# Kernel optimization log

Measured on AMD Instinct MI355X. Metric: run time of the kernel, lower is better.

The kernel has to match this reference:

```python
import jax, jax.numpy as jnp
import numpy as np

DIM = 512
HEADS = 16
WIN = (7, 7)
N = WIN[0] * WIN[1]
B_ = 4096
HEAD_DIM = DIM // HEADS
SCALE = HEAD_DIM ** (-0.5)


def _relative_position_index():
    ch = np.arange(WIN[0])
    cw = np.arange(WIN[1])
    coords = np.stack(np.meshgrid(ch, cw, indexing='ij'))  # (2, Wh, Ww)
    cf = coords.reshape(2, -1)                               # (2, N)
    rel = cf[:, :, None] - cf[:, None, :]                    # (2, N, N)
    rel = rel.transpose(1, 2, 0).astype(np.int32)            # (N, N, 2)
    rel[:, :, 0] += WIN[0] - 1
    rel[:, :, 1] += WIN[1] - 1
    rel[:, :, 0] *= 2 * WIN[1] - 1
    return jnp.asarray(rel.sum(-1))                          # (N, N) int32


def setup_inputs() -> dict:
    key = jax.random.key(0)
    ks = jax.random.split(key, 6)
    x = jax.random.normal(ks[0], (B_, N, DIM), dtype=jnp.float32)
    qkv_w = jax.random.normal(ks[1], (3 * DIM, DIM), dtype=jnp.float32) * (DIM ** -0.5)
    qkv_b = jnp.zeros((3 * DIM,), dtype=jnp.float32)
    proj_w = jax.random.normal(ks[2], (DIM, DIM), dtype=jnp.float32) * (DIM ** -0.5)
    proj_b = jnp.zeros((DIM,), dtype=jnp.float32)
    n_rel = (2 * WIN[0] - 1) * (2 * WIN[1] - 1)  # 169
    bias_table = jax.random.normal(ks[3], (n_rel, HEADS), dtype=jnp.float32) * 0.02
    rel_idx = _relative_position_index()
    return {"x": x, "qkv_w": qkv_w, "qkv_b": qkv_b, "proj_w": proj_w,
            "proj_b": proj_b, "bias_table": bias_table, "rel_idx": rel_idx}


def reference(x, qkv_w, qkv_b, proj_w, proj_b, bias_table, rel_idx):
    B, n, C = x.shape
    # qkv projection: (B, N, 3C) -> (3, B, H, N, hd)
    qkv = x @ qkv_w.T + qkv_b
    qkv = qkv.reshape(B, n, 3, HEADS, HEAD_DIM).transpose(2, 0, 3, 1, 4)
    q, k, v = qkv[0], qkv[1], qkv[2]
    q = q * SCALE
    attn = jnp.einsum('bhnd,bhmd->bhnm', q, k)               # (B, H, N, N)
    # gather relative position bias: (N*N, H) -> (H, N, N)
    bias = bias_table[rel_idx.reshape(-1)].reshape(n, n, HEADS).transpose(2, 0, 1)
    attn = jax.nn.softmax(attn + bias[None], axis=-1)
    out = jnp.einsum('bhnm,bhmd->bhnd', attn, v)
    out = out.transpose(0, 2, 1, 3).reshape(B, n, C)
    return out @ proj_w.T + proj_b
```

## Files before the change

kernel.cpp:

```cpp
#include <hip/hip_runtime.h>
#include <cstdint>
#include <type_traits>

#define B_WIN 4096
#define NTOK 49
#define DIMC 512
#define HEADS 16
#define HD 32
#define M_ROWS (B_WIN * NTOK)
#define SCALE 0.17677669529663689f

using bf16x8 = __attribute__((ext_vector_type(8))) short;
using f32x4  = __attribute__((ext_vector_type(4))) float;
using u16x8  = __attribute__((ext_vector_type(8))) unsigned short;

__device__ inline unsigned short f2bf(float f) {
    uint32_t u = __float_as_uint(f);
    uint32_t r = (u + 0x7fffu + ((u >> 16) & 1u)) >> 16;
    return (unsigned short)r;
}
__device__ inline unsigned int pk2(float lo, float hi) {
    return (unsigned int)f2bf(lo) | ((unsigned int)f2bf(hi) << 16);
}

__device__ __forceinline__ void gll16(const unsigned short* g, unsigned short* l) {
    __builtin_amdgcn_global_load_lds(
        (const __attribute__((address_space(1))) void*)g,
        (__attribute__((address_space(3))) void*)l, 16, 0, 0);
}

#define DSR(dst, addr) asm volatile("ds_read_b128 %0, %1" : "=v"(dst) : "v"(addr))
#define SCHED0() __builtin_amdgcn_sched_barrier(0)
#define BARRIER() do { SCHED0(); __builtin_amdgcn_s_barrier(); SCHED0(); } while (0)
#define LGKM0() do { asm volatile("s_waitcnt lgkmcnt(0)"); SCHED0(); } while (0)

__global__ __launch_bounds__(256) void cvt_f32_bf16(
    const float* __restrict__ in, unsigned short* __restrict__ out, int n4)
{
    for (int i = blockIdx.x * blockDim.x + threadIdx.x; i < n4;
         i += gridDim.x * blockDim.x) {
        float4 v = reinterpret_cast<const float4*>(in)[i];
        ushort4 o;
        o.x = f2bf(v.x); o.y = f2bf(v.y); o.z = f2bf(v.z); o.w = f2bf(v.w);
        reinterpret_cast<ushort4*>(out)[i] = o;
    }
}

__global__ __launch_bounds__(256) void build_bias(
    const float* __restrict__ btab, const int* __restrict__ ridx,
    float* __restrict__ biasPad)
{
    const int idx = blockIdx.x * 256 + threadIdx.x;
    const int h = idx >> 12, rem = idx & 4095;
    const int i = rem >> 6, j = rem & 63;
    float v = -1e30f;
    if (i < NTOK && j < NTOK) v = btab[ridx[i * NTOK + j] * HEADS + h];
    biasPad[idx] = v;
}

template <int OUTF32>
__global__ __launch_bounds__(512, 2) void gemm8p(
    const unsigned short* __restrict__ A,
    const unsigned short* __restrict__ W,
    const float* __restrict__ bias,
    void* __restrict__ Craw,
    int N, int ntn)
{
    extern __shared__ unsigned short lds[];
    constexpr int K = 512, NT = 8;

    const int nwg = gridDim.x;
    const int bid = blockIdx.x;
    const int wg = (bid & 7) * (nwg >> 3) + (bid >> 3);
    const int tn = wg % ntn, tm = wg / ntn;
    const size_t m0 = (size_t)tm * 256, n0 = (size_t)tn * 256;

    const int t = threadIdx.x;
    const int lane = t & 63, wid = t >> 6;
    const int wm = wid >> 2, wn = wid & 3;
    const int l15 = lane & 15, l4 = lane >> 4;

    const unsigned short* pA[2];
    const unsigned short* pB[2];
    int dA[2], dB[2];
#pragma unroll
    for (int u = 0; u < 2; ++u) {
        const int f = t + u * 512, rl = f >> 3, c = f & 7, g = c ^ (rl & 7);
        const int lrA = (rl & 63) + (rl >> 6) * 128;
        const int lrB = ((rl >> 5) << 6) + (rl & 31);
        pA[u] = A + (m0 + lrA) * K + g * 8;
        pB[u] = W + (n0 + lrB) * K + g * 8;
        dA[u] = lrA * 64 + c * 8;
        dB[u] = 32768 + lrB * 64 + c * 8;
    }
#define STG_A(h, T) { const int _b = ((T) & 1) * 16384, _kt = (T) * 64;      \
    gll16(pA[0] + (h) * 64 * K + _kt, lds + _b + dA[0] + (h) * 4096);        \
    gll16(pA[1] + (h) * 64 * K + _kt, lds + _b + dA[1] + (h) * 4096); }
#define STG_B(h, T) { const int _b = ((T) & 1) * 16384, _kt = (T) * 64;      \
    gll16(pB[0] + (h) * 32 * K + _kt, lds + _b + dB[0] + (h) * 2048);        \
    gll16(pB[1] + (h) * 32 * K + _kt, lds + _b + dB[1] + (h) * 2048); }

    const unsigned lbase = (unsigned)(uintptr_t)lds;
    const unsigned swz = (unsigned)(l15 & 7);
    const unsigned cx0 = ((0u + l4) ^ swz) * 16u;
    const unsigned cx1 = ((4u + l4) ^ swz) * 16u;
    const unsigned arow = (unsigned)(wm * 128 + l15) * 128u;
    const unsigned brow = (unsigned)(wn * 64 + l15) * 128u;

    f32x4 acc[8][4] = {};
    bf16x8 a[4][2], b0[2][2], b1[2][2];

    STG_A(0, 0); STG_B(0, 0); STG_A(1, 0); STG_B(1, 0);
    STG_A(0, 1); STG_B(0, 1); STG_A(1, 1);
    asm volatile("s_waitcnt vmcnt(6)");
    SCHED0();
    BARRIER();

    for (int S = 0; S < NT; ++S) {
        const int bs = S & 1;
        const unsigned ab = lbase + (unsigned)bs * 32768u;
        const unsigned bb = lbase + 65536u + (unsigned)bs * 32768u;

#pragma unroll
        for (int m = 0; m < 4; ++m) {
            DSR(a[m][0], ab + arow + m * 2048u + cx0);
            DSR(a[m][1], ab + arow + m * 2048u + cx1);
        }
#pragma unroll
        for (int n = 0; n < 2; ++n) {
            DSR(b0[n][0], bb + brow + n * 2048u + cx0);
            DSR(b0[n][1], bb + brow + n * 2048u + cx1);
        }
        if (S + 1 < NT) STG_B(1, S + 1);
        BARRIER(); LGKM0();
        __builtin_amdgcn_s_setprio(1);
#pragma unroll
        for (int m = 0; m < 4; ++m)
#pragma unroll
            for (int n = 0; n < 2; ++n)
#pragma unroll
                for (int ks = 0; ks < 2; ++ks)
                    acc[m][n] = __builtin_amdgcn_mfma_f32_16x16x32_bf16(
                        a[m][ks], b0[n][ks], acc[m][n], 0, 0, 0);
        __builtin_amdgcn_s_setprio(0);
        BARRIER();

#pragma unroll
        for (int n = 0; n < 2; ++n) {
            DSR(b1[n][0], bb + brow + (n + 2) * 2048u + cx0);
            DSR(b1[n][1], bb + brow + (n + 2) * 2048u + cx1);
        }
        if (S + 2 < NT) STG_A(0, S + 2);
        BARRIER(); LGKM0();
        __builtin_amdgcn_s_setprio(1);
#pragma unroll
        for (int m = 0; m < 4; ++m)
#pragma unroll
            for (int n = 0; n < 2; ++n)
#pragma unroll
                for (int ks = 0; ks < 2; ++ks)
                    acc[m][n + 2] = __builtin_amdgcn_mfma_f32_16x16x32_bf16(
                        a[m][ks], b1[n][ks], acc[m][n + 2], 0, 0, 0);
        __builtin_amdgcn_s_setprio(0);
        BARRIER();

#pragma unroll
        for (int m = 0; m < 4; ++m) {
            DSR(a[m][0], ab + arow + 8192u + m * 2048u + cx0);
            DSR(a[m][1], ab + arow + 8192u + m * 2048u + cx1);
        }
        if (S + 2 < NT) STG_B(0, S + 2);
        BARRIER(); LGKM0();
        __builtin_amdgcn_s_setprio(1);
#pragma unroll
        for (int m = 0; m < 4; ++m)
#pragma unroll
            for (int n = 0; n < 2; ++n)
#pragma unroll
                for (int ks = 0; ks < 2; ++ks)
                    acc[m + 4][n] = __builtin_amdgcn_mfma_f32_16x16x32_bf16(
                        a[m][ks], b0[n][ks], acc[m + 4][n], 0, 0, 0);
        __builtin_amdgcn_s_setprio(0);
        BARRIER();

        if (S + 2 < NT) STG_A(1, S + 2);
        if (S < NT - 2)       { asm volatile("s_waitcnt vmcnt(6)"); SCHED0(); }
        else if (S == NT - 2) { asm volatile("s_waitcnt vmcnt(0)"); SCHED0(); }
        BARRIER();
        __builtin_amdgcn_s_setprio(1);
#pragma unroll
        for (int m = 0; m < 4; ++m)
#pragma unroll
            for (int n = 0; n < 2; ++n)
#pragma unroll
                for (int ks = 0; ks < 2; ++ks)
                    acc[m + 4][n + 2] = __builtin_amdgcn_mfma_f32_16x16x32_bf16(
                        a[m][ks], b1[n][ks], acc[m + 4][n + 2], 0, 0, 0);
        __builtin_amdgcn_s_setprio(0);
        BARRIER();
    }

#pragma unroll
    for (int m = 0; m < 8; ++m) {
#pragma unroll
        for (int n = 0; n < 4; ++n) {
            const size_t col = n0 + wn * 64 + n * 16 + l15;
            const float bv = bias[col];
#pragma unroll
            for (int r = 0; r < 4; ++r) {
                const size_t row = m0 + wm * 128 + m * 16 + l4 * 4 + r;
                const float v = acc[m][n][r] + bv;
                if constexpr (OUTF32)
                    ((float*)Craw)[row * N + col] = v;
                else
                    ((unsigned short*)Craw)[row * N + col] = f2bf(v);
            }
        }
    }
#undef STG_A
#undef STG_B
}

__global__ __launch_bounds__(256) void attn_mfma(
    const unsigned short* __restrict__ qkv,
    const float* __restrict__ biasPad,
    unsigned short* __restrict__ attn_out)
{
    __shared__ unsigned short vtile[4][32][72];

    const int w = threadIdx.x >> 6;
    const int g = blockIdx.x * 4 + w;
    const int b = g >> 4, h = g & 15;
    const int lane = threadIdx.x & 63;
    const int l15 = lane & 15, l4 = lane >> 4;

    bf16x8 aq[4], bk[4], vload[4];
#pragma unroll
    for (int mt = 0; mt < 4; ++mt) {
        const int tok = mt * 16 + l15;
        bf16x8 zq = {}, zk = {}, zv = {};
        if (tok < NTOK) {
            const unsigned short* base =
                qkv + (size_t)(b * NTOK + tok) * 1536 + h * HD + l4 * 8;
            zq = *(const bf16x8*)base;
            zk = *(const bf16x8*)(base + 512);
            zv = *(const bf16x8*)(base + 1024);
        }
        aq[mt] = zq; bk[mt] = zk; vload[mt] = zv;
    }

#pragma unroll
    for (int mt = 0; mt < 4; ++mt) {
        const int tok = mt * 16 + l15;
#pragma unroll
        for (int e = 0; e < 8; ++e)
            vtile[w][l4 * 8 + e][tok] = (unsigned short)vload[mt][e];
    }

    f32x4 sacc[4][4] = {};
#pragma unroll
    for (int nt = 0; nt < 4; ++nt)
#pragma unroll
        for (int mt = 0; mt < 4; ++mt)
            sacc[nt][mt] = __builtin_amdgcn_mfma_f32_16x16x32_bf16(
                bk[nt], aq[mt], sacc[nt][mt], 0, 0, 0);

    const float* bb = biasPad + (h << 12);
    unsigned int pw[4][4][2];
#pragma unroll
    for (int mt = 0; mt < 4; ++mt) {
        const int i = mt * 16 + l15;
        const float* brow = bb + i * 64 + l4 * 4;
        float mx = -3.0e38f;
#pragma unroll
        for (int nt = 0; nt < 4; ++nt) {
            const float4 b4 = *(const float4*)(brow + nt * 16);
            const float v0 = fmaf(sacc[nt][mt][0], SCALE, b4.x);
            const float v1 = fmaf(sacc[nt][mt][1], SCALE, b4.y);
            const float v2 = fmaf(sacc[nt][mt][2], SCALE, b4.z);
            const float v3 = fmaf(sacc[nt][mt][3], SCALE, b4.w);
            sacc[nt][mt][0] = v0; sacc[nt][mt][1] = v1;
            sacc[nt][mt][2] = v2; sacc[nt][mt][3] = v3;
            mx = fmaxf(mx, fmaxf(fmaxf(v0, v1), fmaxf(v2, v3)));
        }
        mx = fmaxf(mx, __shfl_xor(mx, 16));
        mx = fmaxf(mx, __shfl_xor(mx, 32));
        float sum = 0.f;
#pragma unroll
        for (int nt = 0; nt < 4; ++nt) {
            const float e0 = __expf(sacc[nt][mt][0] - mx);
            const float e1 = __expf(sacc[nt][mt][1] - mx);
            const float e2 = __expf(sacc[nt][mt][2] - mx);
            const float e3 = __expf(sacc[nt][mt][3] - mx);
            sacc[nt][mt][0] = e0; sacc[nt][mt][1] = e1;
            sacc[nt][mt][2] = e2; sacc[nt][mt][3] = e3;
            sum += (e0 + e1) + (e2 + e3);
        }
        sum += __shfl_xor(sum, 16);
        sum += __shfl_xor(sum, 32);
        const float inv = 1.0f / sum;
#pragma unroll
        for (int nt = 0; nt < 4; ++nt) {
            pw[mt][nt][0] = pk2(sacc[nt][mt][0] * inv, sacc[nt][mt][1] * inv);
            pw[mt][nt][1] = pk2(sacc[nt][mt][2] * inv, sacc[nt][mt][3] * inv);
        }
    }

    bf16x8 ap[4][2];
#pragma unroll
    for (int mt = 0; mt < 4; ++mt)
#pragma unroll
        for (int ks = 0; ks < 2; ++ks) {
            union { int wv[4]; bf16x8 v; } u;
#pragma unroll
            for (int q = 0; q < 4; ++q) {
                const int src = l15 + ((2 * (l4 & 1) + (q >> 1)) << 4);
                const int va = __shfl((int)pw[mt][2 * ks][q & 1], src);
                const int vb = __shfl((int)pw[mt][2 * ks + 1][q & 1], src);
                u.wv[q] = (l4 & 2) ? vb : va;
            }
            ap[mt][ks] = u.v;
        }

    bf16x8 bv2[2][2];
#pragma unroll
    for (int n = 0; n < 2; ++n)
#pragma unroll
        for (int ks = 0; ks < 2; ++ks)
            bv2[n][ks] = *(const bf16x8*)&vtile[w][n * 16 + l15][ks * 32 + l4 * 8];

    f32x4 oacc[4][2] = {};
#pragma unroll
    for (int mt = 0; mt < 4; ++mt)
#pragma unroll
        for (int n = 0; n < 2; ++n)
#pragma unroll
            for (int ks = 0; ks < 2; ++ks)
                oacc[mt][n] = __builtin_amdgcn_mfma_f32_16x16x32_bf16(
                    ap[mt][ks], bv2[n][ks], oacc[mt][n], 0, 0, 0);

#pragma unroll
    for (int mt = 0; mt < 4; ++mt) {
#pragma unroll
        for (int r = 0; r < 4; ++r) {
            const int i = mt * 16 + l4 * 4 + r;
            if (i < NTOK) {
                unsigned short* op =
                    attn_out + (size_t)(b * NTOK + i) * DIMC + h * HD + l15;
                op[0]  = f2bf(oacc[mt][0][r]);
                op[16] = f2bf(oacc[mt][1][r]);
            }
        }
    }
}

extern "C" void kernel_launch(void* const* d_in, const int* in_sizes, int n_in,
                              void* d_out, int out_size, void* d_ws, size_t ws_size,
                              hipStream_t stream)
{
    const float* x      = (const float*)d_in[0];
    const float* qkv_w  = (const float*)d_in[1];
    const float* qkv_b  = (const float*)d_in[2];
    const float* proj_w = (const float*)d_in[3];
    const float* proj_b = (const float*)d_in[4];
    const float* btab   = (const float*)d_in[5];
    const int*   ridx   = (const int*)d_in[6];
    float* out = (float*)d_out;

    char* w = (char*)d_ws;
    const size_t SZ_XBF   = (size_t)M_ROWS * DIMC * 2;
    const size_t SZ_QKVW  = (size_t)1536 * 512 * 2;
    const size_t SZ_PROJW = (size_t)512 * 512 * 2;
    const size_t SZ_BIAS  = (size_t)HEADS * 64 * 64 * 4;
    const size_t SZ_QKV   = (size_t)M_ROWS * 1536 * 2;
    unsigned short* x_bf     = (unsigned short*)w;
    unsigned short* qkvw_bf  = (unsigned short*)(w + SZ_XBF);
    unsigned short* projw_bf = (unsigned short*)(w + SZ_XBF + SZ_QKVW);
    float*          biasPad  = (float*)(w + SZ_XBF + SZ_QKVW + SZ_PROJW);
    unsigned short* qkv      = (unsigned short*)(w + SZ_XBF + SZ_QKVW + SZ_PROJW + SZ_BIAS);
    unsigned short* attn_out = (unsigned short*)((char*)qkv + SZ_QKV);

    hipFuncSetAttribute(reinterpret_cast<const void*>(&gemm8p<0>),
                        hipFuncAttributeMaxDynamicSharedMemorySize, 131072);
    hipFuncSetAttribute(reinterpret_cast<const void*>(&gemm8p<1>),
                        hipFuncAttributeMaxDynamicSharedMemorySize, 131072);

    cvt_f32_bf16<<<4096, 256, 0, stream>>>(x, x_bf, M_ROWS * DIMC / 4);
    cvt_f32_bf16<<<128, 256, 0, stream>>>(qkv_w, qkvw_bf, 1536 * 512 / 4);
    cvt_f32_bf16<<<64, 256, 0, stream>>>(proj_w, projw_bf, 512 * 512 / 4);
    build_bias<<<256, 256, 0, stream>>>(btab, ridx, biasPad);

    gemm8p<0><<<4704, 512, 131072, stream>>>(
        x_bf, qkvw_bf, qkv_b, qkv, 1536, 6);

    attn_mfma<<<16384, 256, 0, stream>>>(qkv, biasPad, attn_out);

    gemm8p<1><<<1568, 512, 131072, stream>>>(
        attn_out, projw_bf, proj_b, out, 512, 2);
}
```

Before: 942.1 us.

## Fuse window attention with output projection in one per-window kernel

Replaces the separate attention kernel and the projection GEMM with one kernel where each 512-thread block handles one window. Each wave computes two heads and writes the bf16 attention output into LDS. The block then runs the 64x512x512 projection against proj weights streamed through LDS double buffers and writes fp32 output with the bias added. This removes the global round trip of the intermediate attention tensor and one launch. In exchange, every block re-streams the full projection weight (relying on L2), runs a small per-block GEMM, and needs about 129KB of LDS, which limits occupancy.

```diff
diff --git a/kernel.cpp b/kernel.cpp
--- a/kernel.cpp
+++ b/kernel.cpp
@@ -33,6 +33,7 @@
 #define SCHED0() __builtin_amdgcn_sched_barrier(0)
 #define BARRIER() do { SCHED0(); __builtin_amdgcn_s_barrier(); SCHED0(); } while (0)
 #define LGKM0() do { asm volatile("s_waitcnt lgkmcnt(0)"); SCHED0(); } while (0)
+#define VMCNT(n) do { asm volatile("s_waitcnt vmcnt(" #n ")"); SCHED0(); } while (0)
 
 __global__ __launch_bounds__(256) void cvt_f32_bf16(
     const float* __restrict__ in, unsigned short* __restrict__ out, int n4)
@@ -112,8 +113,7 @@
 
     STG_A(0, 0); STG_B(0, 0); STG_A(1, 0); STG_B(1, 0);
     STG_A(0, 1); STG_B(0, 1); STG_A(1, 1);
-    asm volatile("s_waitcnt vmcnt(6)");
-    SCHED0();
+    VMCNT(6);
     BARRIER();
 
     for (int S = 0; S < NT; ++S) {
@@ -184,8 +184,8 @@
         BARRIER();
 
         if (S + 2 < NT) STG_A(1, S + 2);
-        if (S < NT - 2)       { asm volatile("s_waitcnt vmcnt(6)"); SCHED0(); }
-        else if (S == NT - 2) { asm volatile("s_waitcnt vmcnt(0)"); SCHED0(); }
+        if (S < NT - 2)       { VMCNT(6); }
+        else if (S == NT - 2) { VMCNT(0); }
         BARRIER();
         __builtin_amdgcn_s_setprio(1);
 #pragma unroll
@@ -221,134 +221,199 @@
 #undef STG_B
 }
 
-__global__ __launch_bounds__(256) void attn_mfma(
+__global__ __launch_bounds__(512, 2) void attn_proj(
     const unsigned short* __restrict__ qkv,
     const float* __restrict__ biasPad,
-    unsigned short* __restrict__ attn_out)
+    const unsigned short* __restrict__ projw,
+    const float* __restrict__ proj_b,
+    float* __restrict__ out)
 {
-    __shared__ unsigned short vtile[4][32][72];
-
-    const int w = threadIdx.x >> 6;
-    const int g = blockIdx.x * 4 + w;
-    const int b = g >> 4, h = g & 15;
-    const int lane = threadIdx.x & 63;
+    extern __shared__ unsigned short lds[];
+    unsigned short* attnrow = lds;
+    const int b = blockIdx.x;
+    const int t = threadIdx.x, w = t >> 6, lane = t & 63;
     const int l15 = lane & 15, l4 = lane >> 4;
-
-    bf16x8 aq[4], bk[4], vload[4];
-#pragma unroll
-    for (int mt = 0; mt < 4; ++mt) {
-        const int tok = mt * 16 + l15;
-        bf16x8 zq = {}, zk = {}, zv = {};
-        if (tok < NTOK) {
-            const unsigned short* base =
-                qkv + (size_t)(b * NTOK + tok) * 1536 + h * HD + l4 * 8;
-            zq = *(const bf16x8*)base;
-            zk = *(const bf16x8*)(base + 512);
-            zv = *(const bf16x8*)(base + 1024);
-        }
-        aq[mt] = zq; bk[mt] = zk; vload[mt] = zv;
-    }
-
-#pragma unroll
-    for (int mt = 0; mt < 4; ++mt) {
-        const int tok = mt * 16 + l15;
-#pragma unroll
-        for (int e = 0; e < 8; ++e)
-            vtile[w][l4 * 8 + e][tok] = (unsigned short)vload[mt][e];
-    }
-
-    f32x4 sacc[4][4] = {};
-#pragma unroll
-    for (int nt = 0; nt < 4; ++nt)
+    unsigned short* vt = lds + 33280 + w * 2304;
+
+    for (int hh = 0; hh < 2; ++hh) {
+        const int h = w * 2 + hh;
+
+        bf16x8 aq[4], bk[4], vload[4];
+#pragma unroll
+        for (int mt = 0; mt < 4; ++mt) {
+            const int tok = mt * 16 + l15;
+            bf16x8 zq = {}, zk = {}, zv = {};
+            if (tok < NTOK) {
+                const unsigned short* base =
+                    qkv + (size_t)(b * NTOK + tok) * 1536 + h * HD + l4 * 8;
+                zq = *(const bf16x8*)base;
+                zk = *(const bf16x8*)(base + 512);
+                zv = *(const bf16x8*)(base + 1024);
+            }
+            aq[mt] = zq; bk[mt] = zk; vload[mt] = zv;
+        }
+
+#pragma unroll
+        for (int mt = 0; mt < 4; ++mt) {
+            const int tok = mt * 16 + l15;
+#pragma unroll
+            for (int e = 0; e < 8; ++e)
+                vt[(l4 * 8 + e) * 72 + tok] = (unsigned short)vload[mt][e];
+        }
+
+        f32x4 sacc[4][4] = {};
+#pragma unroll
+        for (int nt = 0; nt < 4; ++nt)
+#pragma unroll
+            for (int mt = 0; mt < 4; ++mt)
+                sacc[nt][mt] = __builtin_amdgcn_mfma_f32_16x16x32_bf16(
+                    bk[nt], aq[mt], sacc[nt][mt], 0, 0, 0);
+
+        const float* bb = biasPad + (h << 12);
+        unsigned int pw[4][4][2];
+#pragma unroll
+        for (int mt = 0; mt < 4; ++mt) {
+            const int i = mt * 16 + l15;
+            const float* brow = bb + i * 64 + l4 * 4;
+            float mx = -3.0e38f;
+#pragma unroll
+            for (int nt = 0; nt < 4; ++nt) {
+                const float4 b4 = *(const float4*)(brow + nt * 16);
+                const float v0 = fmaf(sacc[nt][mt][0], SCALE, b4.x);
+                const float v1 = fmaf(sacc[nt][mt][1], SCALE, b4.y);
+                const float v2 = fmaf(sacc[nt][mt][2], SCALE, b4.z);
+                const float v3 = fmaf(sacc[nt][mt][3], SCALE, b4.w);
+                sacc[nt][mt][0] = v0; sacc[nt][mt][1] = v1;
+                sacc[nt][mt][2] = v2; sacc[nt][mt][3] = v3;
+                mx = fmaxf(mx, fmaxf(fmaxf(v0, v1), fmaxf(v2, v3)));
+            }
+            mx = fmaxf(mx, __shfl_xor(mx, 16));
+            mx = fmaxf(mx, __shfl_xor(mx, 32));
+            float sum = 0.f;
+#pragma unroll
+            for (int nt = 0; nt < 4; ++nt) {
+                const float e0 = __expf(sacc[nt][mt][0] - mx);
+                const float e1 = __expf(sacc[nt][mt][1] - mx);
+                const float e2 = __expf(sacc[nt][mt][2] - mx);
+                const float e3 = __expf(sacc[nt][mt][3] - mx);
+                sacc[nt][mt][0] = e0; sacc[nt][mt][1] = e1;
+                sacc[nt][mt][2] = e2; sacc[nt][mt][3] = e3;
+                sum += (e0 + e1) + (e2 + e3);
+            }
+            sum += __shfl_xor(sum, 16);
+            sum += __shfl_xor(sum, 32);
+            const float inv = 1.0f / sum;
+#pragma unroll
+            for (int nt = 0; nt < 4; ++nt) {
+                pw[mt][nt][0] = pk2(sacc[nt][mt][0] * inv, sacc[nt][mt][1] * inv);
+                pw[mt][nt][1] = pk2(sacc[nt][mt][2] * inv, sacc[nt][mt][3] * inv);
+            }
+        }
+
+        bf16x8 ap[4][2];
 #pragma unroll
         for (int mt = 0; mt < 4; ++mt)
-            sacc[nt][mt] = __builtin_amdgcn_mfma_f32_16x16x32_bf16(
-                bk[nt], aq[mt], sacc[nt][mt], 0, 0, 0);
-
-    const float* bb = biasPad + (h << 12);
-    unsigned int pw[4][4][2];
-#pragma unroll
-    for (int mt = 0; mt < 4; ++mt) {
-        const int i = mt * 16 + l15;
-        const float* brow = bb + i * 64 + l4 * 4;
-        float mx = -3.0e38f;
-#pragma unroll
-        for (int nt = 0; nt < 4; ++nt) {
-            const float4 b4 = *(const float4*)(brow + nt * 16);
-            const float v0 = fmaf(sacc[nt][mt][0], SCALE, b4.x);
-            const float v1 = fmaf(sacc[nt][mt][1], SCALE, b4.y);
-            const float v2 = fmaf(sacc[nt][mt][2], SCALE, b4.z);
-            const float v3 = fmaf(sacc[nt][mt][3], SCALE, b4.w);
-            sacc[nt][mt][0] = v0; sacc[nt][mt][1] = v1;
-            sacc[nt][mt][2] = v2; sacc[nt][mt][3] = v3;
-            mx = fmaxf(mx, fmaxf(fmaxf(v0, v1), fmaxf(v2, v3)));
-        }
-        mx = fmaxf(mx, __shfl_xor(mx, 16));
-        mx = fmaxf(mx, __shfl_xor(mx, 32));
-        float sum = 0.f;
-#pragma unroll
-        for (int nt = 0; nt < 4; ++nt) {
-            const float e0 = __expf(sacc[nt][mt][0] - mx);
-            const float e1 = __expf(sacc[nt][mt][1] - mx);
-            const float e2 = __expf(sacc[nt][mt][2] - mx);
-            const float e3 = __expf(sacc[nt][mt][3] - mx);
-            sacc[nt][mt][0] = e0; sacc[nt][mt][1] = e1;
-            sacc[nt][mt][2] = e2; sacc[nt][mt][3] = e3;
-            sum += (e0 + e1) + (e2 + e3);
-        }
-        sum += __shfl_xor(sum, 16);
-        sum += __shfl_xor(sum, 32);
-        const float inv = 1.0f / sum;
-#pragma unroll
-        for (int nt = 0; nt < 4; ++nt) {
-            pw[mt][nt][0] = pk2(sacc[nt][mt][0] * inv, sacc[nt][mt][1] * inv);
-            pw[mt][nt][1] = pk2(sacc[nt][mt][2] * inv, sacc[nt][mt][3] * inv);
-        }
-    }
-
-    bf16x8 ap[4][2];
-#pragma unroll
-    for (int mt = 0; mt < 4; ++mt)
-#pragma unroll
-        for (int ks = 0; ks < 2; ++ks) {
-            union { int wv[4]; bf16x8 v; } u;
-#pragma unroll
-            for (int q = 0; q < 4; ++q) {
-                const int src = l15 + ((2 * (l4 & 1) + (q >> 1)) << 4);
-                const int va = __shfl((int)pw[mt][2 * ks][q & 1], src);
-                const int vb = __shfl((int)pw[mt][2 * ks + 1][q & 1], src);
-                u.wv[q] = (l4 & 2) ? vb : va;
-            }
-            ap[mt][ks] = u.v;
-        }
-
-    bf16x8 bv2[2][2];
-#pragma unroll
-    for (int n = 0; n < 2; ++n)
-#pragma unroll
-        for (int ks = 0; ks < 2; ++ks)
-            bv2[n][ks] = *(const bf16x8*)&vtile[w][n * 16 + l15][ks * 32 + l4 * 8];
-
-    f32x4 oacc[4][2] = {};
-#pragma unroll
-    for (int mt = 0; mt < 4; ++mt)
+#pragma unroll
+            for (int ks = 0; ks < 2; ++ks) {
+                union { int wv[4]; bf16x8 v; } u;
+#pragma unroll
+                for (int q = 0; q < 4; ++q) {
+                    const int src = l15 + ((2 * (l4 & 1) + (q >> 1)) << 4);
+                    const int va = __shfl((int)pw[mt][2 * ks][q & 1], src);
+                    const int vb = __shfl((int)pw[mt][2 * ks + 1][q & 1], src);
+                    u.wv[q] = (l4 & 2) ? vb : va;
+                }
+                ap[mt][ks] = u.v;
+            }
+
+        bf16x8 bv2[2][2];
 #pragma unroll
         for (int n = 0; n < 2; ++n)
 #pragma unroll
             for (int ks = 0; ks < 2; ++ks)
-                oacc[mt][n] = __builtin_amdgcn_mfma_f32_16x16x32_bf16(
-                    ap[mt][ks], bv2[n][ks], oacc[mt][n], 0, 0, 0);
-
-#pragma unroll
-    for (int mt = 0; mt < 4; ++mt) {
+                bv2[n][ks] = *(const bf16x8*)&vt[(n * 16 + l15) * 72 +
+                                                 ks * 32 + l4 * 8];
+
+        f32x4 oacc[4][2] = {};
+#pragma unroll
+        for (int mt = 0; mt < 4; ++mt)
+#pragma unroll
+            for (int n = 0; n < 2; ++n)
+#pragma unroll
+                for (int ks = 0; ks < 2; ++ks)
+                    oacc[mt][n] = __builtin_amdgcn_mfma_f32_16x16x32_bf16(
+                        ap[mt][ks], bv2[n][ks], oacc[mt][n], 0, 0, 0);
+
+#pragma unroll
+        for (int mt = 0; mt < 4; ++mt) {
+#pragma unroll
+            for (int r = 0; r < 4; ++r) {
+                const int i = mt * 16 + l4 * 4 + r;
+                attnrow[i * 520 + h * 32 + l15]      = f2bf(oacc[mt][0][r]);
+                attnrow[i * 520 + h * 32 + 16 + l15] = f2bf(oacc[mt][1][r]);
+            }
+        }
+    }
+
+    float pb[4];
+#pragma unroll
+    for (int n = 0; n < 4; ++n) pb[n] = proj_b[w * 64 + n * 16 + l15];
+    LGKM0();
+    BARRIER();
+    VMCNT(0);
+
+#define STG_P(c) {                                                           \
+    unsigned short* _dst = lds + 33280 + (((c) & 1) << 14);                  \
+    _Pragma("unroll") for (int u = 0; u < 4; ++u)                            \
+        gll16(projw + (size_t)t * 512 + (c) * 32 + u * 8,                    \
+              _dst + u * 4096 + t * 8); }
+
+    const unsigned lbase = (unsigned)(uintptr_t)lds;
+
+    STG_P(0); STG_P(1);
+    VMCNT(4);
+    BARRIER();
+
+    f32x4 acc2[4][4] = {};
+    bf16x8 a2[4], b2[4];
+
+#pragma unroll
+    for (int c = 0; c < 16; ++c) {
+#pragma unroll
+        for (int m = 0; m < 4; ++m)
+            DSR(a2[m], lbase + (unsigned)((m * 16 + l15) * 1040 +
+                                          c * 64 + l4 * 16));
+#pragma unroll
+        for (int n = 0; n < 4; ++n)
+            DSR(b2[n], lbase + 66560u + (unsigned)(((c & 1) << 15) +
+                       l4 * 8192 + (w * 64 + n * 16 + l15) * 16));
+        LGKM0();
+        BARRIER();
+        if (c + 2 < 16) STG_P(c + 2);
+        if (c < 14)       { VMCNT(4); }
+        else if (c == 14) { VMCNT(0); }
+        BARRIER();
+        __builtin_amdgcn_s_setprio(1);
+#pragma unroll
+        for (int m = 0; m < 4; ++m)
+#pragma unroll
+            for (int n = 0; n < 4; ++n)
+                acc2[m][n] = __builtin_amdgcn_mfma_f32_16x16x32_bf16(
+                    a2[m], b2[n], acc2[m][n], 0, 0, 0);
+        __builtin_amdgcn_s_setprio(0);
+    }
+#undef STG_P
+
+#pragma unroll
+    for (int m = 0; m < 4; ++m) {
 #pragma unroll
         for (int r = 0; r < 4; ++r) {
-            const int i = mt * 16 + l4 * 4 + r;
+            const int i = m * 16 + l4 * 4 + r;
             if (i < NTOK) {
-                unsigned short* op =
-                    attn_out + (size_t)(b * NTOK + i) * DIMC + h * HD + l15;
-                op[0]  = f2bf(oacc[mt][0][r]);
-                op[16] = f2bf(oacc[mt][1][r]);
+                float* op = out + ((size_t)b * NTOK + i) * DIMC + w * 64 + l15;
+#pragma unroll
+                for (int n = 0; n < 4; ++n)
+                    op[n * 16] = acc2[m][n][r] + pb[n];
             }
         }
     }
@@ -372,18 +437,16 @@
     const size_t SZ_QKVW  = (size_t)1536 * 512 * 2;
     const size_t SZ_PROJW = (size_t)512 * 512 * 2;
     const size_t SZ_BIAS  = (size_t)HEADS * 64 * 64 * 4;
-    const size_t SZ_QKV   = (size_t)M_ROWS * 1536 * 2;
     unsigned short* x_bf     = (unsigned short*)w;
     unsigned short* qkvw_bf  = (unsigned short*)(w + SZ_XBF);
     unsigned short* projw_bf = (unsigned short*)(w + SZ_XBF + SZ_QKVW);
     float*          biasPad  = (float*)(w + SZ_XBF + SZ_QKVW + SZ_PROJW);
     unsigned short* qkv      = (unsigned short*)(w + SZ_XBF + SZ_QKVW + SZ_PROJW + SZ_BIAS);
-    unsigned short* attn_out = (unsigned short*)((char*)qkv + SZ_QKV);
 
     hipFuncSetAttribute(reinterpret_cast<const void*>(&gemm8p<0>),
                         hipFuncAttributeMaxDynamicSharedMemorySize, 131072);
-    hipFuncSetAttribute(reinterpret_cast<const void*>(&gemm8p<1>),
-                        hipFuncAttributeMaxDynamicSharedMemorySize, 131072);
+    hipFuncSetAttribute(reinterpret_cast<const void*>(&attn_proj),
+                        hipFuncAttributeMaxDynamicSharedMemorySize, 132096);
 
     cvt_f32_bf16<<<4096, 256, 0, stream>>>(x, x_bf, M_ROWS * DIMC / 4);
     cvt_f32_bf16<<<128, 256, 0, stream>>>(qkv_w, qkvw_bf, 1536 * 512 / 4);
@@ -393,8 +456,6 @@
     gemm8p<0><<<4704, 512, 131072, stream>>>(
         x_bf, qkvw_bf, qkv_b, qkv, 1536, 6);
 
-    attn_mfma<<<16384, 256, 0, stream>>>(qkv, biasPad, attn_out);
-
-    gemm8p<1><<<1568, 512, 131072, stream>>>(
-        attn_out, projw_bf, proj_b, out, 512, 2);
-}
+    attn_proj<<<4096, 512, 132096, stream>>>(
+        qkv, biasPad, projw_bf, proj_b, out);
+}
```

Result: slower. 1.169 ms (+24.1%).
